# Performance work log

Measured on AMD Instinct MI355X. Metric: run time of the kernel, lower is better.

Reference implementation:

```python
import jax, jax.numpy as jnp
import numpy as np
import math

# --- config (matches init_kwargs) ---
C = 128          # sphere_channels (multiplicity per l)
LMAX = 2
H = 8            # attention heads
B = 16           # graphs per batch (uniform)
M = 512          # nodes per graph
N = B * M        # 8192 nodes
E = 262144       # edges
D = C * sum(2 * l + 1 for l in range(LMAX + 1))  # 1152
_INV_SQRT_C = 1.0 / math.sqrt(C)


def irreps_linear(x, W):
    """e3nn o3.Linear irreps_node->irreps_node: per-l channel mixing, shared over m.
    x: [N, D], W: [LMAX+1, C, C]."""
    outs = []
    s = 0
    for l in range(LMAX + 1):
        d = 2 * l + 1
        blk = x[:, s:s + C * d].reshape(-1, C, d)          # [N, C, 2l+1]
        y = jnp.einsum('ncm,oc->nom', blk, W[l]) * _INV_SQRT_C
        outs.append(y.reshape(-1, C * d))
        s += C * d
    return jnp.concatenate(outs, axis=1)


def init_edge_rot_mat(edge_vec, edge_rand):
    """Faithful port of init_edge_rot_mat; edge_rand plays the role of rand_like."""
    dist = jnp.sqrt(jnp.sum(edge_vec ** 2, axis=1, keepdims=True))
    nx_ = edge_vec / dist
    e2 = edge_rand - 0.5
    e2 = e2 / jnp.sqrt(jnp.sum(e2 ** 2, axis=1, keepdims=True))
    e2b = jnp.stack([-e2[:, 1], e2[:, 0], e2[:, 2]], axis=1)
    e2c = jnp.stack([e2[:, 0], -e2[:, 2], e2[:, 1]], axis=1)
    dot = lambda a: jnp.abs(jnp.sum(a * nx_, axis=1, keepdims=True))
    vdb, vdc = dot(e2b), dot(e2c)
    e2 = jnp.where(dot(e2) > vdb, e2b, e2)
    e2 = jnp.where(dot(e2) > vdc, e2c, e2)
    nz = jnp.cross(nx_, e2)
    nz = nz / jnp.sqrt(jnp.sum(nz ** 2, axis=1, keepdims=True))
    ny = jnp.cross(nx_, nz)
    ny = ny / jnp.sqrt(jnp.sum(ny ** 2, axis=1, keepdims=True))
    rot_inv = jnp.stack([nz, nx_, -ny], axis=2)  # columns [z, x, -y]
    return jnp.transpose(rot_inv, (0, 2, 1))     # [E, 3, 3]


def setup_inputs() -> dict:
    key = jax.random.key(0)
    ks = jax.random.split(key, 10)
    node_features = jax.random.normal(ks[0], (N, D), dtype=jnp.float32)
    edge_vec = jax.random.normal(ks[1], (E, 3), dtype=jnp.float32)
    edge_rand = jax.random.uniform(ks[2], (E, 3), dtype=jnp.float32)
    edge_index = jax.random.randint(ks[3], (2, E), 0, N, dtype=jnp.int32)
    batch = jnp.repeat(jnp.arange(B, dtype=jnp.int32), M)
    W_q = jax.random.normal(ks[4], (LMAX + 1, C, C), dtype=jnp.float32)
    W_k = jax.random.normal(ks[5], (LMAX + 1, C, C), dtype=jnp.float32)
    W_v = jax.random.normal(ks[6], (LMAX + 1, C, C), dtype=jnp.float32)
    W_o = jax.random.normal(ks[7], (LMAX + 1, C, C), dtype=jnp.float32)
    gamma = jnp.ones((C,), dtype=jnp.float32)
    beta = jnp.zeros((C,), dtype=jnp.float32)
    return dict(node_features=node_features, edge_vec=edge_vec, edge_rand=edge_rand,
                W_q=W_q, W_k=W_k, W_v=W_v, W_o=W_o, gamma=gamma, beta=beta,
                edge_index=edge_index, batch=batch)


def reference(node_features, edge_vec, edge_rand, W_q, W_k, W_v, W_o, gamma, beta,
              edge_index, batch):
    # 1) per-edge rotation matrices (detached in the original)
    rot = jax.lax.stop_gradient(init_edge_rot_mat(edge_vec, edge_rand))

    x = node_features  # [N, D] equivariant irreps features

    # 2) SO2EquivariantGraphAttention: irreps q/k/v, dense per-graph multi-head attn
    q = irreps_linear(x, W_q)
    k = irreps_linear(x, W_k)
    v = irreps_linear(x, W_v)
    hd = D // H
    scale = 1.0 / math.sqrt(hd)
    # to_dense_batch with uniform graph sizes == reshape; mask all-true
    qd = q.reshape(B, M, H, hd).transpose(0, 2, 1, 3)  # [B,H,M,hd]
    kd = k.reshape(B, M, H, hd).transpose(0, 2, 1, 3)
    vd = v.reshape(B, M, H, hd).transpose(0, 2, 1, 3)
    scores = jnp.einsum('bhqd,bhkd->bhqk', qd, kd) * scale
    attn_w = jax.nn.softmax(scores, axis=-1)
    o = jnp.einsum('bhqk,bhkd->bhqd', attn_w, vd)
    o = o.transpose(0, 2, 1, 3).reshape(N, D)
    attn_out = irreps_linear(o, W_o)

    # residual connection
    x = x + attn_out

    # 3) EquivariantLayerNormV2: LayerNorm over l=0 dims only (first C)
    inv = x[:, :C]
    mu = jnp.mean(inv, axis=-1, keepdims=True)
    var = jnp.var(inv, axis=-1, keepdims=True)
    inv = (inv - mu) / jnp.sqrt(var + 1e-5) * gamma + beta

    # 4) S2Activation: SiLU on scalar (l=0) components, identity elsewhere
    inv = jax.nn.silu(inv)
    out = jnp.concatenate([inv, x[:, C:]], axis=1)
    return out, rot
```

## Files before the change

### kernel.cpp

```cpp
#include <hip/hip_runtime.h>
#include <hip/hip_bf16.h>

#define C_CH   128
#define DROW   1152
#define NNODE  8192
#define BATCH  16
#define MSEQ   512
#define NHEAD  8
#define HD     144
#define NEDGE  262144

typedef unsigned short ushort_t;
typedef __attribute__((ext_vector_type(8))) short bf16x8;
typedef __attribute__((ext_vector_type(4))) float f32x4;

__device__ __forceinline__ ushort_t f2bu(float x) {
    __hip_bfloat16 h = __float2bfloat16(x);
    return *reinterpret_cast<ushort_t*>(&h);
}
__device__ __forceinline__ float bu2f(ushort_t u) {
    return __bfloat162float(*reinterpret_cast<__hip_bfloat16*>(&u));
}
__device__ __forceinline__ unsigned u16of(const uint4 v, int ii) {
    const unsigned w = ((ii >> 1) == 0) ? v.x : ((ii >> 1) == 1) ? v.y :
                       ((ii >> 1) == 2) ? v.z : v.w;
    return (ii & 1) ? (w >> 16) : (w & 0xFFFFu);
}

#define KP2 136

template<int DL, int NPB, typename TX, typename TY>
__global__ __launch_bounds__(256) void lin_ovl(
    const TX* __restrict__ X,
    const float* __restrict__ W0, const float* __restrict__ W1,
    const float* __restrict__ W2,
    TY* __restrict__ Y0, TY* __restrict__ Y1, TY* __restrict__ Y2,
    const float* __restrict__ resid,
    int baseoff)
{
    constexpr int COLS = NPB * DL;
    constexpr int CT   = COLS / 16;
    __shared__ __align__(16) ushort_t Bs[COLS][KP2];

    const int tid  = threadIdx.x;
    const int wave = tid >> 6;
    const int lane = tid & 63;
    const int l15  = lane & 15;
    const int quad = lane >> 4;
    const int n0   = blockIdx.x * NPB;
    const int z    = blockIdx.y;

    const float* W = (z == 0) ? W0 : (z == 1 ? W1 : W2);
    TY* Y          = (z == 0) ? Y0 : (z == 1 ? Y1 : Y2);

    if constexpr (sizeof(TX) == 4) {
        for (int e4 = tid; e4 < NPB * 32 * DL; e4 += 256) {
            const int nb = e4 / (32 * DL);
            const int rr = (e4 - nb * (32 * DL)) * 4;
            const float4 xv = *reinterpret_cast<const float4*>(
                &X[(size_t)(n0 + nb) * DROW + baseoff + rr]);
            #pragma unroll
            for (int j = 0; j < 4; ++j) {
                const int r = rr + j, c = r / DL, m = r - c * DL;
                Bs[nb * DL + m][c] = f2bu(reinterpret_cast<const float*>(&xv)[j]);
            }
        }
    } else {
        for (int e8 = tid; e8 < NPB * 16 * DL; e8 += 256) {
            const int nb = e8 / (16 * DL);
            const int rr = (e8 - nb * (16 * DL)) * 8;
            const uint4 xv = *reinterpret_cast<const uint4*>(
                &X[(size_t)(n0 + nb) * DROW + baseoff + rr]);
            const ushort_t* xs = reinterpret_cast<const ushort_t*>(&xv);
            #pragma unroll
            for (int j = 0; j < 8; ++j) {
                const int r = rr + j, c = r / DL, m = r - c * DL;
                Bs[nb * DL + m][c] = xs[j];
            }
        }
    }

    const float s = 0.08838834764831845f;

    bf16x8 aw[2][4];
    #pragma unroll
    for (int ot = 0; ot < 2; ++ot)
        #pragma unroll
        for (int kst = 0; kst < 4; ++kst) {
            const float* wp = &W[(size_t)(32 * wave + 16 * ot + l15) * 128 + kst * 32 + quad * 8];
            const float4 wa = *reinterpret_cast<const float4*>(wp);
            const float4 wb = *reinterpret_cast<const float4*>(wp + 4);
            ushort_t t[8] = {f2bu(wa.x), f2bu(wa.y), f2bu(wa.z), f2bu(wa.w),
                             f2bu(wb.x), f2bu(wb.y), f2bu(wb.z), f2bu(wb.w)};
            aw[ot][kst] = *reinterpret_cast<const bf16x8*>(t);
        }

    __syncthreads();

    f32x4 acc[CT][2];
    #pragma unroll
    for (int ct = 0; ct < CT; ++ct) {
        acc[ct][0] = (f32x4){0.f, 0.f, 0.f, 0.f};
        acc[ct][1] = (f32x4){0.f, 0.f, 0.f, 0.f};
    }
    #pragma unroll
    for (int kst = 0; kst < 4; ++kst)
        #pragma unroll
        for (int ct = 0; ct < CT; ++ct) {
            const bf16x8 b = *reinterpret_cast<const bf16x8*>(
                &Bs[ct * 16 + l15][kst * 32 + quad * 8]);
            acc[ct][0] = __builtin_amdgcn_mfma_f32_16x16x32_bf16(aw[0][kst], b, acc[ct][0], 0, 0, 0);
            acc[ct][1] = __builtin_amdgcn_mfma_f32_16x16x32_bf16(aw[1][kst], b, acc[ct][1], 0, 0, 0);
        }

    __syncthreads();

    #pragma unroll
    for (int ct = 0; ct < CT; ++ct)
        #pragma unroll
        for (int ot = 0; ot < 2; ++ot) {
            ushort_t t[4] = {f2bu(acc[ct][ot][0] * s), f2bu(acc[ct][ot][1] * s),
                             f2bu(acc[ct][ot][2] * s), f2bu(acc[ct][ot][3] * s)};
            *reinterpret_cast<uint2*>(&Bs[ct * 16 + l15][32 * wave + 16 * ot + quad * 4]) =
                *reinterpret_cast<const uint2*>(t);
        }
    __syncthreads();

    for (int e8 = tid; e8 < COLS * 16; e8 += 256) {
        const int nb = e8 / (16 * DL);
        const int r0 = (e8 - nb * (16 * DL)) * 8;
        const size_t ga = (size_t)(n0 + nb) * DROW + baseoff + r0;
        if constexpr (sizeof(TY) == 2) {
            ushort_t t[8];
            #pragma unroll
            for (int j = 0; j < 8; ++j) {
                const int r = r0 + j;
                t[j] = Bs[nb * DL + r % DL][r / DL];
            }
            *reinterpret_cast<uint4*>(&Y[ga]) = *reinterpret_cast<const uint4*>(t);
        } else {
            #pragma unroll
            for (int j4 = 0; j4 < 2; ++j4) {
                const float4 rv = *reinterpret_cast<const float4*>(&resid[ga + j4 * 4]);
                float4 ov;
                #pragma unroll
                for (int j = 0; j < 4; ++j) {
                    const int r = r0 + j4 * 4 + j;
                    reinterpret_cast<float*>(&ov)[j] =
                        bu2f(Bs[nb * DL + r % DL][r / DL]) +
                        reinterpret_cast<const float*>(&rv)[j];
                }
                *reinterpret_cast<float4*>(&((float*)Y)[ga + j4 * 4]) = ov;
            }
        }
    }
}

template<int DL, int NPB, int NZ, int FUSE_LN, typename TX, typename TY>
__global__ __launch_bounds__(256) void lin_mfma(
    const TX* __restrict__ X,
    const float* __restrict__ W0, const float* __restrict__ W1,
    const float* __restrict__ W2,
    TY* __restrict__ Y0, TY* __restrict__ Y1, TY* __restrict__ Y2,
    const float* __restrict__ resid,
    const float* __restrict__ gamma, const float* __restrict__ beta,
    int baseoff)
{
    constexpr int COLS = NPB * DL;
    constexpr int CT   = COLS / 16;
    __shared__ __align__(16) ushort_t Xs[COLS][KP2];
    __shared__ __align__(16) ushort_t Es[COLS][KP2];

    const int tid  = threadIdx.x;
    const int wave = tid >> 6;
    const int lane = tid & 63;
    const int l15  = lane & 15;
    const int quad = lane >> 4;
    const int n0   = blockIdx.x * NPB;

    if constexpr (sizeof(TX) == 4) {
        for (int e4 = tid; e4 < NPB * 32 * DL; e4 += 256) {
            const int nb = e4 / (32 * DL);
            const int rr = (e4 - nb * (32 * DL)) * 4;
            const float4 xv = *reinterpret_cast<const float4*>(
                &X[(size_t)(n0 + nb) * DROW + baseoff + rr]);
            #pragma unroll
            for (int j = 0; j < 4; ++j) {
                const int r = rr + j, c = r / DL, m = r - c * DL;
                Xs[nb * DL + m][c] = f2bu(reinterpret_cast<const float*>(&xv)[j]);
            }
        }
    } else {
        for (int e8 = tid; e8 < NPB * 16 * DL; e8 += 256) {
            const int nb = e8 / (16 * DL);
            const int rr = (e8 - nb * (16 * DL)) * 8;
            const uint4 xv = *reinterpret_cast<const uint4*>(
                &X[(size_t)(n0 + nb) * DROW + baseoff + rr]);
            const ushort_t* xs = reinterpret_cast<const ushort_t*>(&xv);
            #pragma unroll
            for (int j = 0; j < 8; ++j) {
                const int r = rr + j, c = r / DL, m = r - c * DL;
                Xs[nb * DL + m][c] = xs[j];
            }
        }
    }

    const float s = 0.08838834764831845f;

    for (int z = 0; z < NZ; ++z) {
        const float* W = (z == 0) ? W0 : (z == 1 ? W1 : W2);
        TY* Y          = (z == 0) ? Y0 : (z == 1 ? Y1 : Y2);

        bf16x8 aw[2][4];
        #pragma unroll
        for (int ot = 0; ot < 2; ++ot)
            #pragma unroll
            for (int kst = 0; kst < 4; ++kst) {
                const float* wp = &W[(size_t)(32 * wave + 16 * ot + l15) * 128 + kst * 32 + quad * 8];
                const float4 wa = *reinterpret_cast<const float4*>(wp);
                const float4 wb = *reinterpret_cast<const float4*>(wp + 4);
                ushort_t t[8] = {f2bu(wa.x), f2bu(wa.y), f2bu(wa.z), f2bu(wa.w),
                                 f2bu(wb.x), f2bu(wb.y), f2bu(wb.z), f2bu(wb.w)};
                aw[ot][kst] = *reinterpret_cast<const bf16x8*>(t);
            }

        __syncthreads();

        f32x4 acc[CT][2];
        #pragma unroll
        for (int ct = 0; ct < CT; ++ct) {
            acc[ct][0] = (f32x4){0.f, 0.f, 0.f, 0.f};
            acc[ct][1] = (f32x4){0.f, 0.f, 0.f, 0.f};
        }
        #pragma unroll
        for (int kst = 0; kst < 4; ++kst)
            #pragma unroll
            for (int ct = 0; ct < CT; ++ct) {
                const bf16x8 b = *reinterpret_cast<const bf16x8*>(
                    &Xs[ct * 16 + l15][kst * 32 + quad * 8]);
                acc[ct][0] = __builtin_amdgcn_mfma_f32_16x16x32_bf16(aw[0][kst], b, acc[ct][0], 0, 0, 0);
                acc[ct][1] = __builtin_amdgcn_mfma_f32_16x16x32_bf16(aw[1][kst], b, acc[ct][1], 0, 0, 0);
            }

        #pragma unroll
        for (int ct = 0; ct < CT; ++ct)
            #pragma unroll
            for (int ot = 0; ot < 2; ++ot) {
                ushort_t t[4] = {f2bu(acc[ct][ot][0] * s), f2bu(acc[ct][ot][1] * s),
                                 f2bu(acc[ct][ot][2] * s), f2bu(acc[ct][ot][3] * s)};
                *reinterpret_cast<uint2*>(&Es[ct * 16 + l15][32 * wave + 16 * ot + quad * 4]) =
                    *reinterpret_cast<const uint2*>(t);
            }
        __syncthreads();

        if constexpr (FUSE_LN) {
            if (tid < NPB * 4) {
                const int nb = tid >> 2, cc = tid & 3;
                float y[32];
                const float* xr = resid + (size_t)(n0 + nb) * DROW + cc * 32;
                float s1 = 0.f, s2 = 0.f;
                #pragma unroll
                for (int j4 = 0; j4 < 8; ++j4) {
                    const float4 rv = *reinterpret_cast<const float4*>(xr + j4 * 4);
                    #pragma unroll
                    for (int j = 0; j < 4; ++j) {
                        const float v = bu2f(Es[nb][cc * 32 + j4 * 4 + j]) +
                                        reinterpret_cast<const float*>(&rv)[j];
                        y[j4 * 4 + j] = v; s1 += v; s2 += v * v;
                    }
                }
                s1 += __shfl_xor(s1, 1); s2 += __shfl_xor(s2, 1);
                s1 += __shfl_xor(s1, 2); s2 += __shfl_xor(s2, 2);
                const float mean = s1 * (1.0f / 128.0f);
                const float var  = s2 * (1.0f / 128.0f) - mean * mean;
                const float rstd = rsqrtf(var + 1e-5f);
                float* op = (float*)Y + (size_t)(n0 + nb) * DROW + cc * 32;
                #pragma unroll
                for (int j4 = 0; j4 < 8; ++j4) {
                    float4 ov;
                    #pragma unroll
                    for (int j = 0; j < 4; ++j) {
                        const int c = cc * 32 + j4 * 4 + j;
                        float t = (y[j4 * 4 + j] - mean) * rstd * gamma[c] + beta[c];
                        reinterpret_cast<float*>(&ov)[j] = t / (1.0f + __expf(-t));
                    }
                    *reinterpret_cast<float4*>(op + j4 * 4) = ov;
                }
            }
        } else {
            for (int e8 = tid; e8 < COLS * 16; e8 += 256) {
                const int nb = e8 / (16 * DL);
                const int r0 = (e8 - nb * (16 * DL)) * 8;
                const size_t ga = (size_t)(n0 + nb) * DROW + baseoff + r0;
                if constexpr (sizeof(TY) == 2) {
                    ushort_t t[8];
                    #pragma unroll
                    for (int j = 0; j < 8; ++j) {
                        const int r = r0 + j;
                        t[j] = Es[nb * DL + r % DL][r / DL];
                    }
                    *reinterpret_cast<uint4*>(&Y[ga]) = *reinterpret_cast<const uint4*>(t);
                } else {
                    #pragma unroll
                    for (int j4 = 0; j4 < 2; ++j4) {
                        const float4 rv = *reinterpret_cast<const float4*>(&resid[ga + j4 * 4]);
                        float4 ov;
                        #pragma unroll
                        for (int j = 0; j < 4; ++j) {
                            const int r = r0 + j4 * 4 + j;
                            reinterpret_cast<float*>(&ov)[j] =
                                bu2f(Es[nb * DL + r % DL][r / DL]) +
                                reinterpret_cast<const float*>(&rv)[j];
                        }
                        *reinterpret_cast<float4*>(&((float*)Y)[ga + j4 * 4]) = ov;
                    }
                }
            }
        }
    }
}

#define KPAD  168
#define VROWS 160
#define VPAD2 72
#define PPAD  68

__global__ __launch_bounds__(256, 2) void attn_kernel(
    const __hip_bfloat16* __restrict__ Q, const __hip_bfloat16* __restrict__ K,
    const __hip_bfloat16* __restrict__ V, __hip_bfloat16* __restrict__ O)
{
    __shared__ __align__(16) ushort_t ksqs[64][KPAD];
    __shared__ __align__(16) ushort_t vst[VROWS][VPAD2];
    __shared__ __align__(16) ushort_t ps[128][PPAD];

    const int tid  = threadIdx.x;
    const int wave = tid >> 6;
    const int lane = tid & 63;
    const int l15  = lane & 15;
    const int quad = lane >> 4;

    const int bid = blockIdx.x;
    const int xcd = bid & 7;
    const int j   = bid >> 3;
    const int bh  = xcd * 16 + (j >> 2);
    const int q0  = (j & 3) * 128;
    const int h   = bh & 7;
    const int b   = bh >> 3;
    const size_t rowbase = (size_t)b * MSEQ * DROW + (size_t)h * HD;
    const float EXSCALE = 0.12022458674074695f;

    const int r0 = tid / 18,          g0 = tid % 18;
    const int r1 = (tid + 256) / 18,  g1 = (tid + 256) % 18;
    const int r2 = (tid + 512) / 18,  g2 = (tid + 512) % 18;
    const int r3 = (tid + 768) / 18,  g3 = (tid + 768) % 18;
    const int r4 = (tid + 1024) / 18, g4 = (tid + 1024) % 18;
    const int ko0 = r0 * DROW + g0 * 8, ko1 = r1 * DROW + g1 * 8;
    const int ko2 = r2 * DROW + g2 * 8, ko3 = r3 * DROW + g3 * 8;
    const int ko4 = r4 * DROW + g4 * 8;
    ushort_t* kld0 = &ksqs[r0][g0 * 8];
    ushort_t* kld1 = &ksqs[r1][g1 * 8];
    ushort_t* kld2 = &ksqs[r2][g2 * 8];
    ushort_t* kld3 = &ksqs[r3][g3 * 8];
    ushort_t* kld4 = &ksqs[r4][g4 * 8];
    const int rqa = tid / 18,          ga = tid % 18;
    const int rqb = (tid + 256) / 18,  gb = (tid + 256) % 18;
    const int voa = (rqa * 4) * DROW + ga * 8;
    const int vob = (rqb * 4) * DROW + gb * 8;
    const int vca = 4 * (rqa ^ ((ga & 3) << 2));
    const int vcb = 4 * (rqb ^ ((gb & 3) << 2));
    const bool hasK4 = (tid < 128);
    const bool hasVB = (tid < 32);

    uint4 kp0, kp1, kp2, kp3, kp4;
    uint4 va0, va1, va2, va3, vb0, vb1, vb2, vb3;

#define LOAD_K(KC) do { \
        const __hip_bfloat16* kb_ = K + rowbase + (size_t)((KC) * 64) * DROW; \
        kp0 = *reinterpret_cast<const uint4*>(kb_ + ko0); \
        kp1 = *reinterpret_cast<const uint4*>(kb_ + ko1); \
        kp2 = *reinterpret_cast<const uint4*>(kb_ + ko2); \
        kp3 = *reinterpret_cast<const uint4*>(kb_ + ko3); \
        if (hasK4) kp4 = *reinterpret_cast<const uint4*>(kb_ + ko4); \
    } while (0)

#define LOAD_V(KC) do { \
        const __hip_bfloat16* vbp_ = V + rowbase + (size_t)((KC) * 64) * DROW; \
        va0 = *reinterpret_cast<const uint4*>(vbp_ + voa); \
        va1 = *reinterpret_cast<const uint4*>(vbp_ + voa + DROW); \
        va2 = *reinterpret_cast<const uint4*>(vbp_ + voa + 2 * DROW); \
        va3 = *reinterpret_cast<const uint4*>(vbp_ + voa + 3 * DROW); \
        if (hasVB) { \
            vb0 = *reinterpret_cast<const uint4*>(vbp_ + vob); \
            vb1 = *reinterpret_cast<const uint4*>(vbp_ + vob + DROW); \
            vb2 = *reinterpret_cast<const uint4*>(vbp_ + vob + 2 * DROW); \
            vb3 = *reinterpret_cast<const uint4*>(vbp_ + vob + 3 * DROW); \
        } \
    } while (0)

#define WRITE_KV() do { \
        *reinterpret_cast<uint4*>(kld0) = kp0; \
        *reinterpret_cast<uint4*>(kld1) = kp1; \
        *reinterpret_cast<uint4*>(kld2) = kp2; \
        *reinterpret_cast<uint4*>(kld3) = kp3; \
        if (hasK4) *reinterpret_cast<uint4*>(kld4) = kp4; \
        _Pragma("unroll") \
        for (int ii = 0; ii < 8; ++ii) { \
            uint2 pk; \
            pk.x = u16of(va0, ii) | (u16of(va1, ii) << 16); \
            pk.y = u16of(va2, ii) | (u16of(va3, ii) << 16); \
            *reinterpret_cast<uint2*>(&vst[ga * 8 + ii][vca]) = pk; \
        } \
        if (hasVB) { \
            _Pragma("unroll") \
            for (int ii = 0; ii < 8; ++ii) { \
                uint2 pk; \
                pk.x = u16of(vb0, ii) | (u16of(vb1, ii) << 16); \
                pk.y = u16of(vb2, ii) | (u16of(vb3, ii) << 16); \
                *reinterpret_cast<uint2*>(&vst[gb * 8 + ii][vcb]) = pk; \
            } \
        } \
    } while (0)

    LOAD_K(0);
    LOAD_V(0);

    for (int idx = tid; idx < 64 * 16; idx += 256)
        ksqs[idx >> 4][HD + (idx & 15)] = 0;
    for (int idx = tid; idx < 16 * VPAD2; idx += 256)
        vst[144 + idx / VPAD2][idx % VPAD2] = (idx / VPAD2 == 0) ? (ushort_t)0x3F80 : (ushort_t)0;

    bf16x8 aq[2][5];
    for (int hh = 0; hh < 2; ++hh) {
        __syncthreads();
        for (int idx = tid; idx < 64 * 18; idx += 256) {
            const int r = idx / 18, g = idx % 18;
            *reinterpret_cast<uint4*>(&ksqs[r][g * 8]) =
                *reinterpret_cast<const uint4*>(&Q[rowbase + (size_t)(q0 + hh * 64 + r) * DROW + g * 8]);
        }
        __syncthreads();
        if ((wave >> 1) == hh) {
            #pragma unroll
            for (int rt = 0; rt < 2; ++rt)
                #pragma unroll
                for (int kst = 0; kst < 5; ++kst)
                    aq[rt][kst] = *reinterpret_cast<const bf16x8*>(
                        &ksqs[32 * (wave & 1) + rt * 16 + l15][kst * 32 + quad * 8]);
        }
    }

    f32x4 oacc[2][10];
    #pragma unroll
    for (int rt = 0; rt < 2; ++rt)
        #pragma unroll
        for (int nt = 0; nt < 10; ++nt) oacc[rt][nt] = (f32x4){0.f, 0.f, 0.f, 0.f};

    for (int kc = 0; kc < 8; ++kc) {
        __syncthreads();
        WRITE_KV();
        __syncthreads();
        if (kc < 7) LOAD_K(kc + 1);

        f32x4 sc[2][4];
        #pragma unroll
        for (int rt = 0; rt < 2; ++rt)
            #pragma unroll
            for (int kt = 0; kt < 4; ++kt) sc[rt][kt] = (f32x4){0.f, 0.f, 0.f, 0.f};
        #pragma unroll
        for (int kst = 0; kst < 5; ++kst) {
            bf16x8 bk[4];
            #pragma unroll
            for (int kt = 0; kt < 4; ++kt)
                bk[kt] = *reinterpret_cast<const bf16x8*>(
                    &ksqs[kt * 16 + l15][kst * 32 + quad * 8]);
            #pragma unroll
            for (int rt = 0; rt < 2; ++rt)
                #pragma unroll
                for (int kt = 0; kt < 4; ++kt)
                    sc[rt][kt] = __builtin_amdgcn_mfma_f32_16x16x32_bf16(aq[rt][kst], bk[kt], sc[rt][kt], 0, 0, 0);
        }

        if (kc < 7) LOAD_V(kc + 1);

        #pragma unroll
        for (int rt = 0; rt < 2; ++rt)
            #pragma unroll
            for (int kt = 0; kt < 4; ++kt)
                #pragma unroll
                for (int i = 0; i < 4; ++i)
                    ps[32 * wave + 16 * rt + quad * 4 + i][16 * kt + l15] =
                        f2bu(exp2f(sc[rt][kt][i] * EXSCALE));

        #pragma unroll
        for (int kp = 0; kp < 2; ++kp) {
            bf16x8 pa[2];
            #pragma unroll
            for (int rt = 0; rt < 2; ++rt)
                pa[rt] = *reinterpret_cast<const bf16x8*>(
                    &ps[32 * wave + 16 * rt + l15][kp * 32 + quad * 8]);
            #pragma unroll
            for (int nt = 0; nt < 10; ++nt) {
                const int vrow = nt * 16 + l15;
                const int vcol = 4 * ((kp * 8 + quad * 2) ^ (((vrow >> 3) & 3) << 2));
                const bf16x8 bv = *reinterpret_cast<const bf16x8*>(&vst[vrow][vcol]);
                #pragma unroll
                for (int rt = 0; rt < 2; ++rt)
                    oacc[rt][nt] = __builtin_amdgcn_mfma_f32_16x16x32_bf16(pa[rt], bv, oacc[rt][nt], 0, 0, 0);
            }
        }
    }

    #pragma unroll
    for (int rt = 0; rt < 2; ++rt) {
        #pragma unroll
        for (int i = 0; i < 4; ++i) {
            const float l = __shfl(oacc[rt][9][i], lane & 48);
            const float inv = 1.0f / l;
            const int row = q0 + 32 * wave + 16 * rt + quad * 4 + i;
            const size_t rb = rowbase + (size_t)row * DROW;
            #pragma unroll
            for (int nt = 0; nt < 9; ++nt)
                O[rb + nt * 16 + l15] = __float2bfloat16(oacc[rt][nt][i] * inv);
        }
    }
#undef LOAD_K
#undef LOAD_V
#undef WRITE_KV
}

__global__ __launch_bounds__(256) void rot_kernel(
    const float* __restrict__ ev, const float* __restrict__ er,
    float* __restrict__ rot)
{
    const int e = blockIdx.x * 256 + threadIdx.x;
    if (e >= NEDGE) return;
    const float vx = ev[e * 3 + 0], vy = ev[e * 3 + 1], vz = ev[e * 3 + 2];
    const float d = sqrtf(vx * vx + vy * vy + vz * vz);
    const float nx0 = vx / d, nx1 = vy / d, nx2 = vz / d;
    float r0 = er[e * 3 + 0] - 0.5f;
    float r1 = er[e * 3 + 1] - 0.5f;
    float r2 = er[e * 3 + 2] - 0.5f;
    const float rn = sqrtf(r0 * r0 + r1 * r1 + r2 * r2);
    r0 /= rn; r1 /= rn; r2 /= rn;
    const float b0 = -r1, b1 = r0, b2v = r2;
    const float c0 = r0, c1 = -r2, c2 = r1;
    const float vd0 = fabsf(r0 * nx0 + r1 * nx1 + r2 * nx2);
    const float vdb = fabsf(b0 * nx0 + b1 * nx1 + b2v * nx2);
    const float vdc = fabsf(c0 * nx0 + c1 * nx1 + c2 * nx2);
    if (vd0 > vdb) { r0 = b0; r1 = b1; r2 = b2v; }
    const float vd1 = fabsf(r0 * nx0 + r1 * nx1 + r2 * nx2);
    if (vd1 > vdc) { r0 = c0; r1 = c1; r2 = c2; }
    float z0 = nx1 * r2 - nx2 * r1;
    float z1 = nx2 * r0 - nx0 * r2;
    float z2 = nx0 * r1 - nx1 * r0;
    const float zn = sqrtf(z0 * z0 + z1 * z1 + z2 * z2);
    z0 /= zn; z1 /= zn; z2 /= zn;
    float y0 = nx1 * z2 - nx2 * z1;
    float y1 = nx2 * z0 - nx0 * z2;
    float y2 = nx0 * z1 - nx1 * z0;
    const float yn = sqrtf(y0 * y0 + y1 * y1 + y2 * y2);
    y0 /= yn; y1 /= yn; y2 /= yn;
    float* rp = rot + (size_t)e * 9;
    rp[0] = z0;   rp[1] = z1;   rp[2] = z2;
    rp[3] = nx0;  rp[4] = nx1;  rp[5] = nx2;
    rp[6] = -y0;  rp[7] = -y1;  rp[8] = -y2;
}

extern "C" void kernel_launch(void* const* d_in, const int* in_sizes, int n_in,
                              void* d_out, int out_size, void* d_ws, size_t ws_size,
                              hipStream_t stream)
{
    (void)in_sizes; (void)n_in; (void)out_size; (void)ws_size;
    const float* x     = (const float*)d_in[0];
    const float* ev    = (const float*)d_in[1];
    const float* er    = (const float*)d_in[2];
    const float* Wq    = (const float*)d_in[3];
    const float* Wk    = (const float*)d_in[4];
    const float* Wv    = (const float*)d_in[5];
    const float* Wo    = (const float*)d_in[6];
    const float* gamma = (const float*)d_in[7];
    const float* beta  = (const float*)d_in[8];

    float* out = (float*)d_out;
    float* rot = out + (size_t)NNODE * DROW;

    const size_t ND = (size_t)NNODE * DROW;
    __hip_bfloat16* q = (__hip_bfloat16*)d_ws;
    __hip_bfloat16* k = q + ND;
    __hip_bfloat16* v = k + ND;
    __hip_bfloat16* o = v + ND;

    rot_kernel<<<NEDGE / 256, 256, 0, stream>>>(ev, er, rot);

    lin_ovl<1, 32, float, __hip_bfloat16><<<dim3(NNODE / 32, 3), 256, 0, stream>>>(
        x, Wq, Wk, Wv, q, k, v, nullptr, 0);
    lin_ovl<3, 16, float, __hip_bfloat16><<<dim3(NNODE / 16, 3), 256, 0, stream>>>(
        x, Wq + 16384, Wk + 16384, Wv + 16384, q, k, v, nullptr, 128);
    lin_ovl<5, 16, float, __hip_bfloat16><<<dim3(NNODE / 16, 3), 256, 0, stream>>>(
        x, Wq + 32768, Wk + 32768, Wv + 32768, q, k, v, nullptr, 512);

    attn_kernel<<<(MSEQ / 128) * NHEAD * BATCH, 256, 0, stream>>>(q, k, v, o);

    lin_mfma<1, 32, 1, 1, __hip_bfloat16, float><<<NNODE / 32, 256, 0, stream>>>(
        o, Wo, nullptr, nullptr, out, nullptr, nullptr, x, gamma, beta, 0);
    lin_ovl<3, 16, __hip_bfloat16, float><<<dim3(NNODE / 16, 1), 256, 0, stream>>>(
        o, Wo + 16384, nullptr, nullptr, out, nullptr, nullptr, x, 128);
    lin_ovl<5, 16, __hip_bfloat16, float><<<dim3(NNODE / 16, 1), 256, 0, stream>>>(
        o, Wo + 32768, nullptr, nullptr, out, nullptr, nullptr, x, 512);
}
```

Before: 239.0 us.

## Pre-transpose input to bf16 m-major layout and permute attention output

```diff
diff --git a/kernel.cpp b/kernel.cpp
--- a/kernel.cpp
+++ b/kernel.cpp
@@ -26,12 +26,17 @@
                        ((ii >> 1) == 2) ? v.z : v.w;
     return (ii & 1) ? (w >> 16) : (w & 0xFFFFu);
 }
+__device__ __forceinline__ int permch(int r) {
+    if (r < 128) return r;
+    if (r < 512) { const int t = r - 128; const int c = t / 3, m = t - c * 3; return 128 + m * 128 + c; }
+    const int t = r - 512; const int c = t / 5, m = t - c * 5; return 512 + m * 128 + c;
+}
 
 #define KP2 136
 
-template<int DL, int NPB, typename TX, typename TY>
+template<int DL, int NPB, typename TY>
 __global__ __launch_bounds__(256) void lin_ovl(
-    const TX* __restrict__ X,
+    const __hip_bfloat16* __restrict__ X,
     const float* __restrict__ W0, const float* __restrict__ W1,
     const float* __restrict__ W2,
     TY* __restrict__ Y0, TY* __restrict__ Y1, TY* __restrict__ Y2,
@@ -53,31 +58,13 @@
     const float* W = (z == 0) ? W0 : (z == 1 ? W1 : W2);
     TY* Y          = (z == 0) ? Y0 : (z == 1 ? Y1 : Y2);
 
-    if constexpr (sizeof(TX) == 4) {
-        for (int e4 = tid; e4 < NPB * 32 * DL; e4 += 256) {
-            const int nb = e4 / (32 * DL);
-            const int rr = (e4 - nb * (32 * DL)) * 4;
-            const float4 xv = *reinterpret_cast<const float4*>(
-                &X[(size_t)(n0 + nb) * DROW + baseoff + rr]);
-            #pragma unroll
-            for (int j = 0; j < 4; ++j) {
-                const int r = rr + j, c = r / DL, m = r - c * DL;
-                Bs[nb * DL + m][c] = f2bu(reinterpret_cast<const float*>(&xv)[j]);
-            }
-        }
-    } else {
-        for (int e8 = tid; e8 < NPB * 16 * DL; e8 += 256) {
-            const int nb = e8 / (16 * DL);
-            const int rr = (e8 - nb * (16 * DL)) * 8;
-            const uint4 xv = *reinterpret_cast<const uint4*>(
-                &X[(size_t)(n0 + nb) * DROW + baseoff + rr]);
-            const ushort_t* xs = reinterpret_cast<const ushort_t*>(&xv);
-            #pragma unroll
-            for (int j = 0; j < 8; ++j) {
-                const int r = rr + j, c = r / DL, m = r - c * DL;
-                Bs[nb * DL + m][c] = xs[j];
-            }
-        }
+    for (int e = tid; e < COLS * 16; e += 256) {
+        const int row = e >> 4, u = e & 15;
+        const int nb = row / DL, m = row - nb * DL;
+        const __hip_bfloat16* src =
+            X + (size_t)(n0 + nb) * DROW + baseoff + m * 128 + u * 8;
+        *reinterpret_cast<uint4*>(&Bs[row][u * 8]) =
+            *reinterpret_cast<const uint4*>(src);
     }
 
     const float s = 0.08838834764831845f;
@@ -509,6 +496,11 @@
         }
     }
 
+    int pofs[9];
+    #pragma unroll
+    for (int nt = 0; nt < 9; ++nt)
+        pofs[nt] = permch(h * HD + nt * 16 + l15);
+    const size_t nodebase = (size_t)b * MSEQ * DROW;
     #pragma unroll
     for (int rt = 0; rt < 2; ++rt) {
         #pragma unroll
@@ -516,10 +508,10 @@
             const float l = __shfl(oacc[rt][9][i], lane & 48);
             const float inv = 1.0f / l;
             const int row = q0 + 32 * wave + 16 * rt + quad * 4 + i;
-            const size_t rb = rowbase + (size_t)row * DROW;
+            const size_t rb = nodebase + (size_t)row * DROW;
             #pragma unroll
             for (int nt = 0; nt < 9; ++nt)
-                O[rb + nt * 16 + l15] = __float2bfloat16(oacc[rt][nt][i] * inv);
+                O[rb + pofs[nt]] = __float2bfloat16(oacc[rt][nt][i] * inv);
         }
     }
 #undef LOAD_K
@@ -527,11 +519,38 @@
 #undef WRITE_KV
 }
 
-__global__ __launch_bounds__(256) void rot_kernel(
+#define ROT_BLOCKS  (NEDGE / 256)
+#define CONV_BLOCKS 1152
+
+__global__ __launch_bounds__(256) void rot_conv_kernel(
     const float* __restrict__ ev, const float* __restrict__ er,
-    float* __restrict__ rot)
+    float* __restrict__ rot,
+    const float* __restrict__ x, __hip_bfloat16* __restrict__ xb)
 {
-    const int e = blockIdx.x * 256 + threadIdx.x;
+    const int bx = blockIdx.x;
+    if (bx >= ROT_BLOCKS) {
+        const int NTH = CONV_BLOCKS * 256;
+        const int gid = (bx - ROT_BLOCKS) * 256 + threadIdx.x;
+        const int TOT = NNODE * 144;
+        for (int q = gid; q < TOT; q += NTH) {
+            const int node = q / 144, g = q - (q / 144) * 144;
+            const float* xr = x + (size_t)node * DROW;
+            int base, stride;
+            if (g < 16)      { base = g * 8;                    stride = 1; }
+            else if (g < 64) { const int t = (g - 16) * 8; const int m = t >> 7;
+                               base = 128 + (t & 127) * 3 + m;  stride = 3; }
+            else             { const int t = (g - 64) * 8; const int m = t >> 7;
+                               base = 512 + (t & 127) * 5 + m;  stride = 5; }
+            ushort_t tb[8];
+            #pragma unroll
+            for (int jj = 0; jj < 8; ++jj) tb[jj] = f2bu(xr[base + jj * stride]);
+            *reinterpret_cast<uint4*>(
+                reinterpret_cast<ushort_t*>(xb) + (size_t)node * DROW + g * 8) =
+                *reinterpret_cast<const uint4*>(tb);
+        }
+        return;
+    }
+    const int e = bx * 256 + threadIdx.x;
     if (e >= NEDGE) return;
     const float vx = ev[e * 3 + 0], vy = ev[e * 3 + 1], vz = ev[e * 3 + 2];
     const float d = sqrtf(vx * vx + vy * vy + vz * vz);
@@ -588,22 +607,25 @@
     __hip_bfloat16* k = q + ND;
     __hip_bfloat16* v = k + ND;
     __hip_bfloat16* o = v + ND;
-
-    rot_kernel<<<NEDGE / 256, 256, 0, stream>>>(ev, er, rot);
-
-    lin_ovl<1, 32, float, __hip_bfloat16><<<dim3(NNODE / 32, 3), 256, 0, stream>>>(
-        x, Wq, Wk, Wv, q, k, v, nullptr, 0);
-    lin_ovl<3, 16, float, __hip_bfloat16><<<dim3(NNODE / 16, 3), 256, 0, stream>>>(
-        x, Wq + 16384, Wk + 16384, Wv + 16384, q, k, v, nullptr, 128);
-    lin_ovl<5, 16, float, __hip_bfloat16><<<dim3(NNODE / 16, 3), 256, 0, stream>>>(
-        x, Wq + 32768, Wk + 32768, Wv + 32768, q, k, v, nullptr, 512);
+    __hip_bfloat16* xp = o;
+
+    rot_conv_kernel<<<ROT_BLOCKS + CONV_BLOCKS, 256, 0, stream>>>(
+        ev, er, rot, x, xp);
+
+    lin_ovl<1, 32, __hip_bfloat16><<<dim3(NNODE / 32, 3), 256, 0, stream>>>(
+        xp, Wq, Wk, Wv, q, k, v, nullptr, 0);
+    lin_ovl<3, 16, __hip_bfloat16><<<dim3(NNODE / 16, 3), 256, 0, stream>>>(
+        xp, Wq + 16384, Wk + 16384, Wv + 16384, q, k, v, nullptr, 128);
+    lin_ovl<5, 16, __hip_bfloat16><<<dim3(NNODE / 16, 3), 256, 0, stream>>>(
+        xp, Wq + 32768, Wk + 32768, Wv + 32768, q, k, v, nullptr, 512);
 
     attn_kernel<<<(MSEQ / 128) * NHEAD * BATCH, 256, 0, stream>>>(q, k, v, o);
 
     lin_mfma<1, 32, 1, 1, __hip_bfloat16, float><<<NNODE / 32, 256, 0, stream>>>(
         o, Wo, nullptr, nullptr, out, nullptr, nullptr, x, gamma, beta, 0);
-    lin_ovl<3, 16, __hip_bfloat16, float><<<dim3(NNODE / 16, 1), 256, 0, stream>>>(
+
+    lin_ovl<3, 16, float><<<dim3(NNODE / 16, 1), 256, 0, stream>>>(
         o, Wo + 16384, nullptr, nullptr, out, nullptr, nullptr, x, 128);
-    lin_ovl<5, 16, __hip_bfloat16, float><<<dim3(NNODE / 16, 1), 256, 0, stream>>>(
+    lin_ovl<5, 16, float><<<dim3(NNODE / 16, 1), 256, 0, stream>>>(
         o, Wo + 32768, nullptr, nullptr, out, nullptr, nullptr, x, 512);
 }
```

Measured after the change: 256.4 us. +7.2%, slower.
